# Optimization experiments

Measured on AMD Instinct MI355X. Metric: run time of the kernel, lower is better.

Reference implementation:

```python
import jax, jax.numpy as jnp
import numpy as np
from jax import lax

_MAX_SQRT_GRADIENT = 1000.0
B, T, W, LRU_W, H, TW = 32, 2048, 512, 512, 8, 4


@jax.custom_vjp
def sqrt_bound(x):
    return jnp.sqrt(x)

def _sb_fwd(x):
    return jnp.sqrt(x), x

def _sb_bwd(x, g):
    return (g / jnp.sqrt(jnp.clip(4.0 * x, 1.0 / _MAX_SQRT_GRADIENT ** 2)),)

sqrt_bound.defvjp(_sb_fwd, _sb_bwd)


def setup_inputs() -> dict:
    key = jax.random.key(0)
    ks = jax.random.split(key, 8)
    bw = LRU_W // H
    # RG-LRU `A` parameter: uniform on ring [0.9, 0.999], softplus-inverse transform
    rng = np.random.default_rng(0)
    u = rng.uniform(0.9 ** 2 + 1e-8, 0.999 ** 2 + 1e-8, size=(LRU_W,))
    log_a = 0.5 * np.log(u)
    a_param = np.log(np.exp(-log_a) - 1.0).astype(np.float32)
    return dict(
        x=jax.random.normal(ks[0], (B, T, W), jnp.float32),
        reset=jnp.zeros((B, T), jnp.bool_),
        h0=jnp.zeros((B, LRU_W), jnp.float32),
        w_x=jax.random.normal(ks[1], (W, LRU_W), jnp.float32) / np.sqrt(W).astype(np.float32),
        b_x=jnp.zeros((LRU_W,), jnp.float32),
        w_y=jax.random.normal(ks[2], (W, LRU_W), jnp.float32) / np.sqrt(W).astype(np.float32),
        b_y=jnp.zeros((LRU_W,), jnp.float32),
        conv_w=jax.random.normal(ks[3], (TW, LRU_W), jnp.float32) * np.sqrt(0.01 / TW).astype(np.float32),
        conv_b=jnp.zeros((LRU_W,), jnp.float32),
        a_param=jnp.asarray(a_param),
        wi=jax.random.normal(ks[4], (H, bw, bw), jnp.float32) / np.sqrt(bw).astype(np.float32),
        bi=jnp.zeros((H, bw), jnp.float32),
        wa=jax.random.normal(ks[5], (H, bw, bw), jnp.float32) / np.sqrt(bw).astype(np.float32),
        ba=jnp.zeros((H, bw), jnp.float32),
        w_out=jax.random.normal(ks[6], (LRU_W, W), jnp.float32) / np.sqrt(LRU_W).astype(np.float32),
        b_out=jnp.zeros((W,), jnp.float32),
    )


def _block_diag(x, w, b):
    # x: [B,T,(h*i)] ; w: [h,i,j] ; b: [h,j]
    h, bw, _ = w.shape
    xh = x.reshape(x.shape[:-1] + (h, bw))
    y = jnp.einsum('bthi,hij->bthj', xh, w) + b
    return y.reshape(x.shape[:-1] + (h * bw,))


def _causal_conv1d(x, w, b):
    # output[t] = sum_s w[s] * x[t - (TW-1-s)] + b  (left zero-padded)
    tw = w.shape[0]
    t = x.shape[1]
    xp = jnp.pad(x, ((0, 0), (tw - 1, 0), (0, 0)))
    out = jnp.broadcast_to(b, x.shape).astype(x.dtype)
    for s in range(tw):
        out = out + xp[:, s:s + t] * w[s]
    return out


def _forward(x, reset, h0, w_x, b_x, w_y, b_y, conv_w, conv_b, a_param,
             wi, bi, wa, ba, w_out, b_out):
    xb = x @ w_x + b_x                      # [B,T,LRU_W]
    yb = jax.nn.gelu(x @ w_y + b_y)         # tanh-approx gelu, matches torch approximate='tanh'
    xb = _causal_conv1d(xb, conv_w, conv_b)
    # RG-LRU gating
    gate_x = jax.nn.sigmoid(_block_diag(xb, wi, bi))
    gate_a = jax.nn.sigmoid(_block_diag(xb, wa, ba))
    log_a = -8.0 * gate_a * jax.nn.softplus(a_param)
    a = jnp.exp(log_a)
    mult = sqrt_bound(1.0 - jnp.exp(2.0 * log_a))
    mult = jnp.where(reset[..., None], jnp.ones_like(mult), mult)
    normed = xb * gate_x * mult
    a = a * (1.0 - reset[..., None].astype(a.dtype))  # zero `a` at document boundaries

    def step(h, inp):
        a_t, x_t = inp
        h = a_t * h + x_t
        return h, h

    _, ys = lax.scan(step, h0, (jnp.swapaxes(a, 0, 1), jnp.swapaxes(normed, 0, 1)))
    y = jnp.swapaxes(ys, 0, 1)              # [B,T,LRU_W]
    return (y * yb) @ w_out + b_out


def reference(x, reset, h0, w_x, b_x, w_y, b_y, conv_w, conv_b, a_param,
              wi, bi, wa, ba, w_out, b_out):
    return _forward(x, reset, h0, w_x, b_x, w_y, b_y, conv_w, conv_b, a_param,
                    wi, bi, wa, ba, w_out, b_out)
```

## Files before the change

### kernel.cpp

```cpp
#include <hip/hip_runtime.h>

typedef __bf16 bf16x8 __attribute__((ext_vector_type(8)));
typedef float f32x4 __attribute__((ext_vector_type(4)));
typedef unsigned short u16x8 __attribute__((ext_vector_type(8)));
typedef unsigned short u16x4 __attribute__((ext_vector_type(4)));

#define MBY (1ull << 20)

__device__ __forceinline__ unsigned short f2bf(float f) {
  union { float f; unsigned u; } v; v.f = f;
  unsigned r = v.u + 0x7fffu + ((v.u >> 16) & 1u);
  return (unsigned short)(r >> 16);
}
__device__ __forceinline__ float bf2f(unsigned short s) {
  union { unsigned u; float f; } v; v.u = ((unsigned)s) << 16;
  return v.f;
}
__device__ __forceinline__ float fexp(float x) {
  return __builtin_amdgcn_exp2f(x * 1.44269504088896340736f);
}
__device__ __forceinline__ float frcp(float x) {
  return __builtin_amdgcn_rcpf(x);
}
__device__ __forceinline__ void gl2lds16(const void* g, void* l) {
  __builtin_amdgcn_global_load_lds(
      (const __attribute__((address_space(1))) unsigned int*)g,
      (__attribute__((address_space(3))) unsigned int*)l, 16, 0, 0);
}

__global__ void prep_misc_kernel(const float* __restrict__ wx, const float* __restrict__ wy,
                                 const float* __restrict__ wo,
                                 const float* __restrict__ wi, const float* __restrict__ wa,
                                 const float* __restrict__ a_param,
                                 unsigned short* __restrict__ wxT, unsigned short* __restrict__ wyT,
                                 unsigned short* __restrict__ woT,
                                 unsigned short* __restrict__ wiTH, unsigned short* __restrict__ wiTL,
                                 unsigned short* __restrict__ waTH, unsigned short* __restrict__ waTL,
                                 float* __restrict__ spbuf) {
  int bid = blockIdx.x, tid = threadIdx.x;
  if (bid < 3072) {
    int mat = bid >> 10;
    int g = (bid & 1023) * 256 + tid;
    int n = g & 511, k = g >> 9;
    const float* src = (mat == 0) ? wx : (mat == 1) ? wy : wo;
    unsigned short* dst = (mat == 0) ? wxT : (mat == 1) ? wyT : woT;
    dst[(size_t)n * 512 + k] = f2bf(src[(size_t)k * 512 + n]);
  } else if (bid < 3200) {
    int g = (bid - 3072) * 256 + tid;
    int j = g & 63, i = (g >> 6) & 63, h = g >> 12;
    size_t src = (size_t)h * 4096 + (size_t)i * 64 + j;
    size_t dst = (size_t)h * 4096 + (size_t)j * 64 + i;
    float v = wi[src];
    unsigned short hh = f2bf(v);
    wiTH[dst] = hh; wiTL[dst] = f2bf(v - bf2f(hh));
    v = wa[src];
    hh = f2bf(v);
    waTH[dst] = hh; waTL[dst] = f2bf(v - bf2f(hh));
  } else {
    int g = (bid - 3200) * 256 + tid;
    if (g < 512) {
      float ap = a_param[g];
      spbuf[g] = (ap > 0.f) ? ap + log1pf(expf(-ap)) : log1pf(expf(ap));
    }
  }
}

__global__ __launch_bounds__(256, 2)
void gemm_dual_kernel(const float* __restrict__ x,
                      const unsigned short* __restrict__ wxT,
                      const unsigned short* __restrict__ wyT,
                      const float* __restrict__ bx, const float* __restrict__ by,
                      unsigned short* __restrict__ xbp, unsigned short* __restrict__ ybuf) {
  __shared__ __align__(16) unsigned short As[128 * 32];
  __shared__ __align__(16) unsigned short Bs0[128 * 32];
  __shared__ __align__(16) unsigned short Bs1[128 * 32];
  const int tid = threadIdx.x, lane = tid & 63, wv = tid >> 6;
  const int m0 = blockIdx.y * 128, n0 = blockIdx.x * 128;
  const int sr = lane >> 2, sk = (lane & 3) * 8;
  const int wm = (wv >> 1) << 6, wn = (wv & 1) << 6;
  const int fm = lane & 15, fq = lane >> 4;

  f32x4 acc0[4][4], acc1[4][4];
#pragma unroll
  for (int i = 0; i < 4; ++i)
#pragma unroll
    for (int j = 0; j < 4; ++j) {
      acc0[i][j] = f32x4{0.f, 0.f, 0.f, 0.f};
      acc1[i][j] = f32x4{0.f, 0.f, 0.f, 0.f};
    }

  const float* gaf          = x   + (size_t)(m0 + wv * 32 + sr) * 512 + sk;
  const unsigned short* gb0 = wxT + (size_t)(n0 + wv * 32 + sr) * 512 + sk;
  const unsigned short* gb1 = wyT + (size_t)(n0 + wv * 32 + sr) * 512 + sk;
  unsigned short* lA  = &As [wv * 32 * 32];
  unsigned short* lB0 = &Bs0[wv * 32 * 32];
  unsigned short* lB1 = &Bs1[wv * 32 * 32];

  for (int k0 = 0; k0 < 512; k0 += 32) {
    __syncthreads();
    gl2lds16(gb0 + k0,            lB0);
    gl2lds16(gb0 + k0 + 16 * 512, lB0 + 16 * 32);
    gl2lds16(gb1 + k0,            lB1);
    gl2lds16(gb1 + k0 + 16 * 512, lB1 + 16 * 32);
    {
      float4 a0 = *(const float4*)(gaf + k0);
      float4 a1 = *(const float4*)(gaf + k0 + 4);
      float4 a2 = *(const float4*)(gaf + k0 + 16 * 512);
      float4 a3 = *(const float4*)(gaf + k0 + 16 * 512 + 4);
      u16x8 w0, w1;
      w0[0] = f2bf(a0.x); w0[1] = f2bf(a0.y); w0[2] = f2bf(a0.z); w0[3] = f2bf(a0.w);
      w0[4] = f2bf(a1.x); w0[5] = f2bf(a1.y); w0[6] = f2bf(a1.z); w0[7] = f2bf(a1.w);
      w1[0] = f2bf(a2.x); w1[1] = f2bf(a2.y); w1[2] = f2bf(a2.z); w1[3] = f2bf(a2.w);
      w1[4] = f2bf(a3.x); w1[5] = f2bf(a3.y); w1[6] = f2bf(a3.z); w1[7] = f2bf(a3.w);
      *(u16x8*)&lA[sr * 32 + sk]        = w0;
      *(u16x8*)&lA[(sr + 16) * 32 + sk] = w1;
    }
    __syncthreads();
    bf16x8 af[4], bfr0[4], bfr1[4];
#pragma unroll
    for (int i = 0; i < 4; ++i)
      af[i] = *(const bf16x8*)&As[(wm + i * 16 + fm) * 32 + fq * 8];
#pragma unroll
    for (int j = 0; j < 4; ++j) {
      bfr0[j] = *(const bf16x8*)&Bs0[(wn + j * 16 + fm) * 32 + fq * 8];
      bfr1[j] = *(const bf16x8*)&Bs1[(wn + j * 16 + fm) * 32 + fq * 8];
    }
#pragma unroll
    for (int i = 0; i < 4; ++i)
#pragma unroll
      for (int j = 0; j < 4; ++j) {
        acc0[i][j] = __builtin_amdgcn_mfma_f32_16x16x32_bf16(af[i], bfr0[j], acc0[i][j], 0, 0, 0);
        acc1[i][j] = __builtin_amdgcn_mfma_f32_16x16x32_bf16(af[i], bfr1[j], acc1[i][j], 0, 0, 0);
      }
  }
#pragma unroll
  for (int i = 0; i < 4; ++i) {
#pragma unroll
    for (int j = 0; j < 4; ++j) {
      int col = n0 + wn + j * 16 + fm;
      float bxv = bx[col], byv = by[col];
#pragma unroll
      for (int r = 0; r < 4; ++r) {
        int row = m0 + wm + i * 16 + fq * 4 + r;
        size_t idx = (size_t)row * 512 + col;
        xbp[idx] = f2bf(acc0[i][j][r] + bxv);
        float z = acc1[i][j][r] + byv;
        float zc = 0.7978845608028654f * (z + 0.044715f * z * z * z);
        float e = fexp(2.0f * zc);
        float th = 1.0f - 2.0f * frcp(e + 1.0f);
        ybuf[idx] = f2bf(0.5f * z * (1.0f + th));
      }
    }
  }
}

#define XP 72
__global__ __launch_bounds__(256, 2)
void conv_gates_kernel(const unsigned short* __restrict__ xbp,
                       const unsigned char* __restrict__ reset,
                       const float* __restrict__ conv_w, const float* __restrict__ conv_b,
                       const float* __restrict__ spbuf,
                       const unsigned short* __restrict__ wiTH, const unsigned short* __restrict__ wiTL,
                       const unsigned short* __restrict__ waTH, const unsigned short* __restrict__ waTL,
                       const float* __restrict__ bi, const float* __restrict__ ba,
                       unsigned short* __restrict__ aq_out, unsigned short* __restrict__ nrm) {
  __shared__ __align__(16) unsigned short xin[131 * 64];
  __shared__ __align__(16) unsigned short xcH[128 * XP];
  __shared__ __align__(16) unsigned short xcL[128 * XP];
  const int tile = blockIdx.x, h = blockIdx.y, b = blockIdx.z;
  const int t0 = tile << 7;
  const int tid = threadIdx.x, lane = tid & 63, wv = tid >> 6;
  const int fm = lane & 15, fq = lane >> 4;

  const size_t cb0 = ((size_t)b * 2048) * 512 + (h << 6);
  for (int idx = tid; idx < 1048; idx += 256) {
    int row = idx >> 3, c8 = (idx & 7) << 3;
    int t = t0 - 3 + row;
    u16x8 v = u16x8{0, 0, 0, 0, 0, 0, 0, 0};
    if (t >= 0) v = *(const u16x8*)(xbp + cb0 + (size_t)t * 512 + c8);
    *(u16x8*)&xin[row * 64 + c8] = v;
  }
  __syncthreads();
  {
    const int c8 = (tid & 7) << 3, u0 = tid >> 3;
    const int ch8 = (h << 6) + c8;
    float cw[4][8], cbv[8];
#pragma unroll
    for (int s = 0; s < 4; ++s) {
      *(float4*)&cw[s][0] = *(const float4*)(conv_w + s * 512 + ch8);
      *(float4*)&cw[s][4] = *(const float4*)(conv_w + s * 512 + ch8 + 4);
    }
    *(float4*)&cbv[0] = *(const float4*)(conv_b + ch8);
    *(float4*)&cbv[4] = *(const float4*)(conv_b + ch8 + 4);
#pragma unroll
    for (int g = 0; g < 4; ++g) {
      int u = u0 + g * 32;
      u16x8 r0 = *(const u16x8*)&xin[(u + 0) * 64 + c8];
      u16x8 r1 = *(const u16x8*)&xin[(u + 1) * 64 + c8];
      u16x8 r2 = *(const u16x8*)&xin[(u + 2) * 64 + c8];
      u16x8 r3 = *(const u16x8*)&xin[(u + 3) * 64 + c8];
      u16x8 oh, ol;
#pragma unroll
      for (int j = 0; j < 8; ++j) {
        float v = cbv[j] + cw[0][j] * bf2f(r0[j]) + cw[1][j] * bf2f(r1[j]) +
                  cw[2][j] * bf2f(r2[j]) + cw[3][j] * bf2f(r3[j]);
        oh[j] = f2bf(v);
        ol[j] = f2bf(v - bf2f(oh[j]));
      }
      *(u16x8*)&xcH[u * XP + c8] = oh;
      *(u16x8*)&xcL[u * XP + c8] = ol;
    }
  }
  bf16x8 bIh[4][2], bIl[4][2], bAh[4][2], bAl[4][2];
#pragma unroll
  for (int nt = 0; nt < 4; ++nt)
#pragma unroll
    for (int ks = 0; ks < 2; ++ks) {
      size_t off = (size_t)h * 4096 + (size_t)(nt * 16 + fm) * 64 + ks * 32 + fq * 8;
      bIh[nt][ks] = *(const bf16x8*)(wiTH + off);
      bIl[nt][ks] = *(const bf16x8*)(wiTL + off);
      bAh[nt][ks] = *(const bf16x8*)(waTH + off);
      bAl[nt][ks] = *(const bf16x8*)(waTL + off);
    }
  f32x4 accI[2][4], accA[2][4];
#pragma unroll
  for (int mt = 0; mt < 2; ++mt)
#pragma unroll
    for (int nt = 0; nt < 4; ++nt) {
      accI[mt][nt] = f32x4{0.f, 0.f, 0.f, 0.f};
      accA[mt][nt] = f32x4{0.f, 0.f, 0.f, 0.f};
    }
  __syncthreads();
#pragma unroll
  for (int mt = 0; mt < 2; ++mt) {
    int mrow = wv * 32 + mt * 16 + fm;
#pragma unroll
    for (int ks = 0; ks < 2; ++ks) {
      bf16x8 ah = *(const bf16x8*)&xcH[mrow * XP + ks * 32 + fq * 8];
      bf16x8 al = *(const bf16x8*)&xcL[mrow * XP + ks * 32 + fq * 8];
#pragma unroll
      for (int nt = 0; nt < 4; ++nt) {
        accI[mt][nt] = __builtin_amdgcn_mfma_f32_16x16x32_bf16(ah, bIh[nt][ks], accI[mt][nt], 0, 0, 0);
        accI[mt][nt] = __builtin_amdgcn_mfma_f32_16x16x32_bf16(ah, bIl[nt][ks], accI[mt][nt], 0, 0, 0);
        accI[mt][nt] = __builtin_amdgcn_mfma_f32_16x16x32_bf16(al, bIh[nt][ks], accI[mt][nt], 0, 0, 0);
        accA[mt][nt] = __builtin_amdgcn_mfma_f32_16x16x32_bf16(ah, bAh[nt][ks], accA[mt][nt], 0, 0, 0);
        accA[mt][nt] = __builtin_amdgcn_mfma_f32_16x16x32_bf16(ah, bAl[nt][ks], accA[mt][nt], 0, 0, 0);
        accA[mt][nt] = __builtin_amdgcn_mfma_f32_16x16x32_bf16(al, bAh[nt][ks], accA[mt][nt], 0, 0, 0);
      }
    }
  }
#pragma unroll
  for (int nt = 0; nt < 4; ++nt) {
    int colg = (h << 6) + nt * 16 + fm;
    float biv = bi[colg], bav = ba[colg];
    float sp8 = -8.0f * spbuf[colg];
#pragma unroll
    for (int mt = 0; mt < 2; ++mt) {
#pragma unroll
      for (int r = 0; r < 4; ++r) {
        int mrow = wv * 32 + mt * 16 + fq * 4 + r;
        int t = t0 + mrow;
        float xcv = bf2f(xcH[mrow * XP + nt * 16 + fm]) + bf2f(xcL[mrow * XP + nt * 16 + fm]);
        float gx = frcp(1.0f + fexp(-(accI[mt][nt][r] + biv)));
        float ga = frcp(1.0f + fexp(-(accA[mt][nt][r] + bav)));
        float la = sp8 * ga;
        float av = fexp(la);
        float mult = __builtin_amdgcn_sqrtf(fmaxf(1.0f - fexp(2.0f * la), 0.0f));
        if (reset[b * 2048 + t]) { mult = 1.0f; av = 0.0f; }
        size_t idx = ((size_t)(b * 2048 + t)) * 512 + colg;
        aq_out[idx] = (unsigned short)fminf(av * 65536.0f + 0.5f, 65535.0f);
        nrm[idx] = f2bf(xcv * gx * mult);
      }
    }
  }
}

__global__ void scan1_kernel(const unsigned short* __restrict__ aq, const unsigned short* __restrict__ nrm,
                             float* __restrict__ cA, float* __restrict__ cH) {
  int g = blockIdx.x * 256 + threadIdx.x;
  int c4 = (g & 127) << 2, k = (g >> 7) & 31, b = g >> 12;
  size_t base = ((size_t)(b * 2048 + k * 64)) * 512 + c4;
  float A[4] = {1.f, 1.f, 1.f, 1.f}, h[4] = {0.f, 0.f, 0.f, 0.f};
#pragma unroll 4
  for (int i = 0; i < 64; ++i) {
    u16x4 av = *(const u16x4*)(aq + base + (size_t)i * 512);
    u16x4 nv = *(const u16x4*)(nrm + base + (size_t)i * 512);
#pragma unroll
    for (int j = 0; j < 4; ++j) {
      float a = (float)av[j] * (1.0f / 65536.0f);
      A[j] *= a;
      h[j] = fmaf(a, h[j], bf2f(nv[j]));
    }
  }
  int ci = ((b * 32 + k) << 9) + c4;
#pragma unroll
  for (int j = 0; j < 4; ++j) { cA[ci + j] = A[j]; cH[ci + j] = h[j]; }
}

__global__ void scan2_kernel(const float* __restrict__ cA, const float* __restrict__ cH,
                             const float* __restrict__ h0, float* __restrict__ hinit) {
  int b = blockIdx.x, c = threadIdx.x;
  float h = h0[b * 512 + c];
  for (int k = 0; k < 32; ++k) {
    int ci = ((b * 32 + k) << 9) + c;
    hinit[ci] = h;
    h = fmaf(cA[ci], h, cH[ci]);
  }
}

__global__ void scan3_kernel(const unsigned short* __restrict__ aq, const unsigned short* __restrict__ nrm,
                             const float* __restrict__ hinit, const unsigned short* __restrict__ ybuf,
                             unsigned short* __restrict__ p) {
  int g = blockIdx.x * 256 + threadIdx.x;
  int c4 = (g & 127) << 2, k = (g >> 7) & 31, b = g >> 12;
  size_t base = ((size_t)(b * 2048 + k * 64)) * 512 + c4;
  int ci = ((b * 32 + k) << 9) + c4;
  float h[4];
#pragma unroll
  for (int j = 0; j < 4; ++j) h[j] = hinit[ci + j];
#pragma unroll 4
  for (int i = 0; i < 64; ++i) {
    u16x4 av = *(const u16x4*)(aq + base + (size_t)i * 512);
    u16x4 nv = *(const u16x4*)(nrm + base + (size_t)i * 512);
    u16x4 yv = *(const u16x4*)(ybuf + base + (size_t)i * 512);
    u16x4 pv;
#pragma unroll
    for (int j = 0; j < 4; ++j) {
      float a = (float)av[j] * (1.0f / 65536.0f);
      h[j] = fmaf(a, h[j], bf2f(nv[j]));
      pv[j] = f2bf(h[j] * bf2f(yv[j]));
    }
    *(u16x4*)(p + base + (size_t)i * 512) = pv;
  }
}

__global__ __launch_bounds__(256, 2)
void gemm_out_kernel(const unsigned short* __restrict__ p,
                     const unsigned short* __restrict__ woT,
                     const float* __restrict__ bout, float* __restrict__ out) {
  __shared__ __align__(16) unsigned short As[128 * 32];
  __shared__ __align__(16) unsigned short Bs[128 * 32];
  const int tid = threadIdx.x, lane = tid & 63, wv = tid >> 6;
  const int m0 = blockIdx.y * 128, n0 = blockIdx.x * 128;
  const int sr = lane >> 2, sk = (lane & 3) * 8;
  const int wm = (wv >> 1) << 6, wn = (wv & 1) << 6;
  const int fm = lane & 15, fq = lane >> 4;

  f32x4 acc[4][4];
#pragma unroll
  for (int i = 0; i < 4; ++i)
#pragma unroll
    for (int j = 0; j < 4; ++j) acc[i][j] = f32x4{0.f, 0.f, 0.f, 0.f};

  const unsigned short* ga = p   + (size_t)(m0 + wv * 32 + sr) * 512 + sk;
  const unsigned short* gb = woT + (size_t)(n0 + wv * 32 + sr) * 512 + sk;
  unsigned short* lA = &As[wv * 32 * 32];
  unsigned short* lB = &Bs[wv * 32 * 32];

  for (int k0 = 0; k0 < 512; k0 += 32) {
    __syncthreads();
    gl2lds16(ga + k0,            lA);
    gl2lds16(ga + k0 + 16 * 512, lA + 16 * 32);
    gl2lds16(gb + k0,            lB);
    gl2lds16(gb + k0 + 16 * 512, lB + 16 * 32);
    __syncthreads();
    bf16x8 af[4], bfr[4];
#pragma unroll
    for (int i = 0; i < 4; ++i)
      af[i] = *(const bf16x8*)&As[(wm + i * 16 + fm) * 32 + fq * 8];
#pragma unroll
    for (int j = 0; j < 4; ++j)
      bfr[j] = *(const bf16x8*)&Bs[(wn + j * 16 + fm) * 32 + fq * 8];
#pragma unroll
    for (int i = 0; i < 4; ++i)
#pragma unroll
      for (int j = 0; j < 4; ++j)
        acc[i][j] = __builtin_amdgcn_mfma_f32_16x16x32_bf16(af[i], bfr[j], acc[i][j], 0, 0, 0);
  }
#pragma unroll
  for (int i = 0; i < 4; ++i) {
#pragma unroll
    for (int j = 0; j < 4; ++j) {
      int col = n0 + wn + j * 16 + fm;
      float bv = bout[col];
#pragma unroll
      for (int r = 0; r < 4; ++r) {
        int row = m0 + wm + i * 16 + fq * 4 + r;
        out[(size_t)row * 512 + col] = acc[i][j][r] + bv;
      }
    }
  }
}

extern "C" void kernel_launch(void* const* d_in, const int* in_sizes, int n_in,
                              void* d_out, int out_size, void* d_ws, size_t ws_size,
                              hipStream_t stream) {
  const float* x             = (const float*)d_in[0];
  const unsigned char* reset = (const unsigned char*)d_in[1];
  const float* h0            = (const float*)d_in[2];
  const float* b_x           = (const float*)d_in[4];
  const float* b_y           = (const float*)d_in[6];
  const float* conv_w        = (const float*)d_in[7];
  const float* conv_b        = (const float*)d_in[8];
  const float* bi            = (const float*)d_in[11];
  const float* ba            = (const float*)d_in[13];
  const float* b_out         = (const float*)d_in[15];

  char* ws = (char*)d_ws;
  unsigned short* xbp  = (unsigned short*)(ws);
  unsigned short* ybuf = (unsigned short*)(ws + 64 * MBY);
  unsigned short* aq   = (unsigned short*)(ws + 128 * MBY);
  unsigned short* nrm  = (unsigned short*)(ws + 192 * MBY);
  float* cA            = (float*)(ws + 256 * MBY);
  float* cH            = (float*)(ws + 258 * MBY);
  float* hinit         = (float*)(ws + 260 * MBY);
  unsigned short* wxT  = (unsigned short*)(ws + 262 * MBY);
  unsigned short* wyT  = (unsigned short*)(ws + 262 * MBY + 524288);
  unsigned short* woT  = (unsigned short*)(ws + 263 * MBY);
  unsigned short* wiTH = (unsigned short*)(ws + 263 * MBY + 524288);
  unsigned short* wiTL = wiTH + 32768;
  unsigned short* waTH = wiTL + 32768;
  unsigned short* waTL = waTH + 32768;
  float* spbuf         = (float*)(waTL + 32768);
  unsigned short* p    = xbp;

  hipLaunchKernelGGL(prep_misc_kernel, dim3(3202), dim3(256), 0, stream,
                     (const float*)d_in[3], (const float*)d_in[5], (const float*)d_in[14],
                     (const float*)d_in[10], (const float*)d_in[12], (const float*)d_in[9],
                     wxT, wyT, woT, wiTH, wiTL, waTH, waTL, spbuf);
  hipLaunchKernelGGL(gemm_dual_kernel, dim3(4, 512), dim3(256), 0, stream,
                     x, wxT, wyT, b_x, b_y, xbp, ybuf);
  hipLaunchKernelGGL(conv_gates_kernel, dim3(16, 8, 32), dim3(256), 0, stream,
                     xbp, reset, conv_w, conv_b, spbuf, wiTH, wiTL, waTH, waTL,
                     bi, ba, aq, nrm);
  hipLaunchKernelGGL(scan1_kernel, dim3(512), dim3(256), 0, stream, aq, nrm, cA, cH);
  hipLaunchKernelGGL(scan2_kernel, dim3(32), dim3(512), 0, stream, cA, cH, h0, hinit);
  hipLaunchKernelGGL(scan3_kernel, dim3(512), dim3(256), 0, stream, aq, nrm, hinit, ybuf, p);
  hipLaunchKernelGGL(gemm_out_kernel, dim3(4, 512), dim3(256), 0, stream, p, woT, b_out, (float*)d_out);
}
```

Measured before the change: 613.0 us.

## Widen GEMM K-step to 64, prefetch x into registers, remap blocks for XCD locality

Both GEMM kernels now load two 32-wide K slices per barrier pair, so a K-loop of 8 iterations replaces 16 and halves the synchronisation count. The dual GEMM also prefetches the next fp32 x tile into registers while the MFMAs for the current tile run. Grids are flattened to 1D with a swizzle that groups blocks landing on the same XCD so they share A rows in cache. The cost is doubled LDS per block and more registers, which may limit the two-blocks-per-CU occupancy.

```diff
diff --git a/kernel.cpp b/kernel.cpp
--- a/kernel.cpp
+++ b/kernel.cpp
@@ -71,11 +71,12 @@
                       const unsigned short* __restrict__ wyT,
                       const float* __restrict__ bx, const float* __restrict__ by,
                       unsigned short* __restrict__ xbp, unsigned short* __restrict__ ybuf) {
-  __shared__ __align__(16) unsigned short As[128 * 32];
-  __shared__ __align__(16) unsigned short Bs0[128 * 32];
-  __shared__ __align__(16) unsigned short Bs1[128 * 32];
+  __shared__ __align__(16) unsigned short As [2 * 128 * 32];
+  __shared__ __align__(16) unsigned short Bs0[2 * 128 * 32];
+  __shared__ __align__(16) unsigned short Bs1[2 * 128 * 32];
   const int tid = threadIdx.x, lane = tid & 63, wv = tid >> 6;
-  const int m0 = blockIdx.y * 128, n0 = blockIdx.x * 128;
+  const int lg = ((blockIdx.x & 7) << 8) | (blockIdx.x >> 3);
+  const int m0 = (lg >> 2) << 7, n0 = (lg & 3) << 7;
   const int sr = lane >> 2, sk = (lane & 3) * 8;
   const int wm = (wv >> 1) << 6, wn = (wv & 1) << 6;
   const int fm = lane & 15, fq = lane >> 4;
@@ -92,46 +93,73 @@
   const float* gaf          = x   + (size_t)(m0 + wv * 32 + sr) * 512 + sk;
   const unsigned short* gb0 = wxT + (size_t)(n0 + wv * 32 + sr) * 512 + sk;
   const unsigned short* gb1 = wyT + (size_t)(n0 + wv * 32 + sr) * 512 + sk;
-  unsigned short* lA  = &As [wv * 32 * 32];
-  unsigned short* lB0 = &Bs0[wv * 32 * 32];
-  unsigned short* lB1 = &Bs1[wv * 32 * 32];
-
-  for (int k0 = 0; k0 < 512; k0 += 32) {
+  unsigned short* lA  = As  + wv * 1024;
+  unsigned short* lB0 = Bs0 + wv * 1024;
+  unsigned short* lB1 = Bs1 + wv * 1024;
+
+  float4 pa[2][4];
+#pragma unroll
+  for (int bb = 0; bb < 2; ++bb) {
+    pa[bb][0] = *(const float4*)(gaf + bb * 32);
+    pa[bb][1] = *(const float4*)(gaf + bb * 32 + 4);
+    pa[bb][2] = *(const float4*)(gaf + bb * 32 + 16 * 512);
+    pa[bb][3] = *(const float4*)(gaf + bb * 32 + 16 * 512 + 4);
+  }
+
+  for (int r = 0; r < 8; ++r) {
+    const int k0 = r << 6;
     __syncthreads();
-    gl2lds16(gb0 + k0,            lB0);
-    gl2lds16(gb0 + k0 + 16 * 512, lB0 + 16 * 32);
-    gl2lds16(gb1 + k0,            lB1);
-    gl2lds16(gb1 + k0 + 16 * 512, lB1 + 16 * 32);
-    {
-      float4 a0 = *(const float4*)(gaf + k0);
-      float4 a1 = *(const float4*)(gaf + k0 + 4);
-      float4 a2 = *(const float4*)(gaf + k0 + 16 * 512);
-      float4 a3 = *(const float4*)(gaf + k0 + 16 * 512 + 4);
+#pragma unroll
+    for (int bb = 0; bb < 2; ++bb) {
+      gl2lds16(gb0 + k0 + bb * 32,            lB0 + bb * 4096);
+      gl2lds16(gb0 + k0 + bb * 32 + 16 * 512, lB0 + bb * 4096 + 512);
+      gl2lds16(gb1 + k0 + bb * 32,            lB1 + bb * 4096);
+      gl2lds16(gb1 + k0 + bb * 32 + 16 * 512, lB1 + bb * 4096 + 512);
       u16x8 w0, w1;
-      w0[0] = f2bf(a0.x); w0[1] = f2bf(a0.y); w0[2] = f2bf(a0.z); w0[3] = f2bf(a0.w);
-      w0[4] = f2bf(a1.x); w0[5] = f2bf(a1.y); w0[6] = f2bf(a1.z); w0[7] = f2bf(a1.w);
-      w1[0] = f2bf(a2.x); w1[1] = f2bf(a2.y); w1[2] = f2bf(a2.z); w1[3] = f2bf(a2.w);
-      w1[4] = f2bf(a3.x); w1[5] = f2bf(a3.y); w1[6] = f2bf(a3.z); w1[7] = f2bf(a3.w);
-      *(u16x8*)&lA[sr * 32 + sk]        = w0;
-      *(u16x8*)&lA[(sr + 16) * 32 + sk] = w1;
+      w0[0] = f2bf(pa[bb][0].x); w0[1] = f2bf(pa[bb][0].y);
+      w0[2] = f2bf(pa[bb][0].z); w0[3] = f2bf(pa[bb][0].w);
+      w0[4] = f2bf(pa[bb][1].x); w0[5] = f2bf(pa[bb][1].y);
+      w0[6] = f2bf(pa[bb][1].z); w0[7] = f2bf(pa[bb][1].w);
+      w1[0] = f2bf(pa[bb][2].x); w1[1] = f2bf(pa[bb][2].y);
+      w1[2] = f2bf(pa[bb][2].z); w1[3] = f2bf(pa[bb][2].w);
+      w1[4] = f2bf(pa[bb][3].x); w1[5] = f2bf(pa[bb][3].y);
+      w1[6] = f2bf(pa[bb][3].z); w1[7] = f2bf(pa[bb][3].w);
+      *(u16x8*)&lA[bb * 4096 + sr * 32 + sk] = w0;
+      *(u16x8*)&lA[bb * 4096 + sr * 32 + sk + 512] = w1;
     }
     __syncthreads();
-    bf16x8 af[4], bfr0[4], bfr1[4];
-#pragma unroll
-    for (int i = 0; i < 4; ++i)
-      af[i] = *(const bf16x8*)&As[(wm + i * 16 + fm) * 32 + fq * 8];
-#pragma unroll
-    for (int j = 0; j < 4; ++j) {
-      bfr0[j] = *(const bf16x8*)&Bs0[(wn + j * 16 + fm) * 32 + fq * 8];
-      bfr1[j] = *(const bf16x8*)&Bs1[(wn + j * 16 + fm) * 32 + fq * 8];
-    }
-#pragma unroll
-    for (int i = 0; i < 4; ++i)
+    if (r < 7) {
+      const float* g2 = gaf + k0 + 64;
+#pragma unroll
+      for (int bb = 0; bb < 2; ++bb) {
+        pa[bb][0] = *(const float4*)(g2 + bb * 32);
+        pa[bb][1] = *(const float4*)(g2 + bb * 32 + 4);
+        pa[bb][2] = *(const float4*)(g2 + bb * 32 + 16 * 512);
+        pa[bb][3] = *(const float4*)(g2 + bb * 32 + 16 * 512 + 4);
+      }
+    }
+#pragma unroll
+    for (int bb = 0; bb < 2; ++bb) {
+      const unsigned short* Ab  = As  + bb * 4096;
+      const unsigned short* B0b = Bs0 + bb * 4096;
+      const unsigned short* B1b = Bs1 + bb * 4096;
+      bf16x8 af[4], bfr0[4], bfr1[4];
+#pragma unroll
+      for (int i = 0; i < 4; ++i)
+        af[i] = *(const bf16x8*)&Ab[(wm + i * 16 + fm) * 32 + fq * 8];
 #pragma unroll
       for (int j = 0; j < 4; ++j) {
-        acc0[i][j] = __builtin_amdgcn_mfma_f32_16x16x32_bf16(af[i], bfr0[j], acc0[i][j], 0, 0, 0);
-        acc1[i][j] = __builtin_amdgcn_mfma_f32_16x16x32_bf16(af[i], bfr1[j], acc1[i][j], 0, 0, 0);
-      }
+        bfr0[j] = *(const bf16x8*)&B0b[(wn + j * 16 + fm) * 32 + fq * 8];
+        bfr1[j] = *(const bf16x8*)&B1b[(wn + j * 16 + fm) * 32 + fq * 8];
+      }
+#pragma unroll
+      for (int i = 0; i < 4; ++i)
+#pragma unroll
+        for (int j = 0; j < 4; ++j) {
+          acc0[i][j] = __builtin_amdgcn_mfma_f32_16x16x32_bf16(af[i], bfr0[j], acc0[i][j], 0, 0, 0);
+          acc1[i][j] = __builtin_amdgcn_mfma_f32_16x16x32_bf16(af[i], bfr1[j], acc1[i][j], 0, 0, 0);
+        }
+    }
   }
 #pragma unroll
   for (int i = 0; i < 4; ++i) {
@@ -338,10 +366,11 @@
 void gemm_out_kernel(const unsigned short* __restrict__ p,
                      const unsigned short* __restrict__ woT,
                      const float* __restrict__ bout, float* __restrict__ out) {
-  __shared__ __align__(16) unsigned short As[128 * 32];
-  __shared__ __align__(16) unsigned short Bs[128 * 32];
+  __shared__ __align__(16) unsigned short As[2 * 128 * 32];
+  __shared__ __align__(16) unsigned short Bs[2 * 128 * 32];
   const int tid = threadIdx.x, lane = tid & 63, wv = tid >> 6;
-  const int m0 = blockIdx.y * 128, n0 = blockIdx.x * 128;
+  const int lg = ((blockIdx.x & 7) << 8) | (blockIdx.x >> 3);
+  const int m0 = (lg >> 2) << 7, n0 = (lg & 3) << 7;
   const int sr = lane >> 2, sk = (lane & 3) * 8;
   const int wm = (wv >> 1) << 6, wn = (wv & 1) << 6;
   const int fm = lane & 15, fq = lane >> 4;
@@ -354,28 +383,37 @@
 
   const unsigned short* ga = p   + (size_t)(m0 + wv * 32 + sr) * 512 + sk;
   const unsigned short* gb = woT + (size_t)(n0 + wv * 32 + sr) * 512 + sk;
-  unsigned short* lA = &As[wv * 32 * 32];
-  unsigned short* lB = &Bs[wv * 32 * 32];
-
-  for (int k0 = 0; k0 < 512; k0 += 32) {
+  unsigned short* lA = As + wv * 1024;
+  unsigned short* lB = Bs + wv * 1024;
+
+  for (int r = 0; r < 8; ++r) {
+    const int k0 = r << 6;
     __syncthreads();
-    gl2lds16(ga + k0,            lA);
-    gl2lds16(ga + k0 + 16 * 512, lA + 16 * 32);
-    gl2lds16(gb + k0,            lB);
-    gl2lds16(gb + k0 + 16 * 512, lB + 16 * 32);
+#pragma unroll
+    for (int bb = 0; bb < 2; ++bb) {
+      gl2lds16(ga + k0 + bb * 32,            lA + bb * 4096);
+      gl2lds16(ga + k0 + bb * 32 + 16 * 512, lA + bb * 4096 + 512);
+      gl2lds16(gb + k0 + bb * 32,            lB + bb * 4096);
+      gl2lds16(gb + k0 + bb * 32 + 16 * 512, lB + bb * 4096 + 512);
+    }
     __syncthreads();
-    bf16x8 af[4], bfr[4];
-#pragma unroll
-    for (int i = 0; i < 4; ++i)
-      af[i] = *(const bf16x8*)&As[(wm + i * 16 + fm) * 32 + fq * 8];
-#pragma unroll
-    for (int j = 0; j < 4; ++j)
-      bfr[j] = *(const bf16x8*)&Bs[(wn + j * 16 + fm) * 32 + fq * 8];
-#pragma unroll
-    for (int i = 0; i < 4; ++i)
+#pragma unroll
+    for (int bb = 0; bb < 2; ++bb) {
+      const unsigned short* Ab = As + bb * 4096;
+      const unsigned short* Bb = Bs + bb * 4096;
+      bf16x8 af[4], bfr[4];
+#pragma unroll
+      for (int i = 0; i < 4; ++i)
+        af[i] = *(const bf16x8*)&Ab[(wm + i * 16 + fm) * 32 + fq * 8];
 #pragma unroll
       for (int j = 0; j < 4; ++j)
-        acc[i][j] = __builtin_amdgcn_mfma_f32_16x16x32_bf16(af[i], bfr[j], acc[i][j], 0, 0, 0);
+        bfr[j] = *(const bf16x8*)&Bb[(wn + j * 16 + fm) * 32 + fq * 8];
+#pragma unroll
+      for (int i = 0; i < 4; ++i)
+#pragma unroll
+        for (int j = 0; j < 4; ++j)
+          acc[i][j] = __builtin_amdgcn_mfma_f32_16x16x32_bf16(af[i], bfr[j], acc[i][j], 0, 0, 0);
+    }
   }
 #pragma unroll
   for (int i = 0; i < 4; ++i) {
@@ -428,7 +466,7 @@
                      (const float*)d_in[3], (const float*)d_in[5], (const float*)d_in[14],
                      (const float*)d_in[10], (const float*)d_in[12], (const float*)d_in[9],
                      wxT, wyT, woT, wiTH, wiTL, waTH, waTL, spbuf);
-  hipLaunchKernelGGL(gemm_dual_kernel, dim3(4, 512), dim3(256), 0, stream,
+  hipLaunchKernelGGL(gemm_dual_kernel, dim3(2048), dim3(256), 0, stream,
                      x, wxT, wyT, b_x, b_y, xbp, ybuf);
   hipLaunchKernelGGL(conv_gates_kernel, dim3(16, 8, 32), dim3(256), 0, stream,
                      xbp, reset, conv_w, conv_b, spbuf, wiTH, wiTL, waTH, waTL,
@@ -436,5 +474,5 @@
   hipLaunchKernelGGL(scan1_kernel, dim3(512), dim3(256), 0, stream, aq, nrm, cA, cH);
   hipLaunchKernelGGL(scan2_kernel, dim3(32), dim3(512), 0, stream, cA, cH, h0, hinit);
   hipLaunchKernelGGL(scan3_kernel, dim3(512), dim3(256), 0, stream, aq, nrm, hinit, ybuf, p);
-  hipLaunchKernelGGL(gemm_out_kernel, dim3(4, 512), dim3(256), 0, stream, p, woT, b_out, (float*)d_out);
-}
+  hipLaunchKernelGGL(gemm_out_kernel, dim3(2048), dim3(256), 0, stream, p, woT, b_out, (float*)d_out);
+}
```

Measured after the change: 588.3 us. 1.04x faster.
